# Performance work log

Measured on AMD Instinct MI355X. Metric: run time of the kernel, lower is better.

## Reference

```python
import jax, jax.numpy as jnp
import numpy as np

DIM = 1024
HEADS = 16
DIM_HEAD = 64
INNER = HEADS * DIM_HEAD  # 1024
SCALE = DIM_HEAD ** -0.5


def setup_inputs() -> dict:
    key = jax.random.key(0)
    ks = jax.random.split(key, 6)
    b, n = 4, 2048
    x = jax.random.normal(ks[0], (b, n, DIM), dtype=jnp.float32)
    gamma = jnp.ones((DIM,), dtype=jnp.float32)
    # weights stored (in, out); torch Linear computes x @ W.T with W (out, in)
    w_q = jax.random.normal(ks[1], (DIM, INNER), dtype=jnp.float32) * (DIM ** -0.5)
    w_kv = jax.random.normal(ks[2], (DIM, 2 * INNER), dtype=jnp.float32) * (DIM ** -0.5)
    w_out = jax.random.normal(ks[3], (INNER, DIM), dtype=jnp.float32) * (INNER ** -0.5)
    null_kv = jax.random.normal(ks[4], (2, HEADS, 1, DIM_HEAD), dtype=jnp.float32)
    return {"x": x, "gamma": gamma, "w_q": w_q, "w_kv": w_kv, "w_out": w_out, "null_kv": null_kv}


def _layer_norm(x, gamma):
    mu = jnp.mean(x, axis=-1, keepdims=True)
    var = jnp.var(x, axis=-1, keepdims=True)
    return (x - mu) * jax.lax.rsqrt(var + 1e-5) * gamma  # beta == 0


def reference(x, gamma, w_q, w_kv, w_out, null_kv):
    b, n, _ = x.shape
    xn = _layer_norm(x, gamma)
    q = xn @ w_q  # [b, n, inner]
    kv = xn @ w_kv
    k, v = jnp.split(kv, 2, axis=-1)
    q = q * SCALE

    def to_heads(t):
        return t.reshape(b, n, HEADS, DIM_HEAD).transpose(0, 2, 1, 3)  # b h n d

    q, k, v = map(to_heads, (q, k, v))
    nk = jnp.broadcast_to(null_kv[0][None], (b, HEADS, 1, DIM_HEAD))
    nv = jnp.broadcast_to(null_kv[1][None], (b, HEADS, 1, DIM_HEAD))
    k = jnp.concatenate([nk, k], axis=2)  # b h (n+1) d
    v = jnp.concatenate([nv, v], axis=2)
    sim = jnp.einsum('bhid,bhjd->bhij', q, k)
    attn = jax.nn.softmax(sim, axis=-1)
    out = jnp.einsum('bhij,bhjd->bhid', attn, v)
    out = out.transpose(0, 2, 1, 3).reshape(b, n, INNER)
    return out @ w_out
```

## Files before the change

kernel.cpp:

```cpp
#include <hip/hip_runtime.h>

typedef unsigned short ushort_t;
using f32x4   = __attribute__((ext_vector_type(4))) float;
using bf16x8  = __attribute__((ext_vector_type(8))) __bf16;
using bf16x4  = __attribute__((ext_vector_type(4))) __bf16;
using short4_t = __attribute__((ext_vector_type(4))) short;
using u32x2   = __attribute__((ext_vector_type(2))) unsigned;

typedef __attribute__((address_space(1))) const void gvoid_t;
typedef __attribute__((address_space(3))) void svoid_t;

union Frag {
    uint4    u4;
    bf16x8   b;
    ushort_t s[8];
};
union Frag2 {
    u32x2    u2;
    bf16x4   b;
    short4_t s4;
    unsigned u[2];
};

__device__ __forceinline__ ushort_t f2bf(float f) {
    union { float f; unsigned u; } a; a.f = f;
    unsigned u = a.u;
    unsigned r = (u + 0x7fffu + ((u >> 16) & 1u)) >> 16;
    return (ushort_t)r;
}
__device__ __forceinline__ float bf2f(ushort_t b) {
    union { unsigned u; float f; } a; a.u = ((unsigned)b) << 16;
    return a.f;
}
__device__ __forceinline__ unsigned pack2bf(float lo, float hi) {
    union { __bf16 h[2]; unsigned u; } p;
    p.h[0] = (__bf16)lo;
    p.h[1] = (__bf16)hi;
    return p.u;
}
__device__ __forceinline__ float exp2_fast(float x) {
#if __has_builtin(__builtin_amdgcn_exp2f)
    return __builtin_amdgcn_exp2f(x);
#else
    return exp2f(x);
#endif
}
__device__ __forceinline__ f32x4 mfma16(Frag2 a, Frag2 b, f32x4 c) {
#if __has_builtin(__builtin_amdgcn_mfma_f32_16x16x16_bf16)
    return __builtin_amdgcn_mfma_f32_16x16x16_bf16(a.b, b.b, c, 0, 0, 0);
#elif __has_builtin(__builtin_amdgcn_mfma_f32_16x16x16bf16_1k)
    return __builtin_amdgcn_mfma_f32_16x16x16bf16_1k(a.s4, b.s4, c, 0, 0, 0);
#else
    f32x4 d;
    asm("v_mfma_f32_16x16x16_bf16 %0, %1, %2, %3"
        : "=v"(d) : "v"(a.u2), "v"(b.u2), "v"(c));
    return d;
#endif
}

#define QSCALE 0.18033688011112042f

__global__ __launch_bounds__(256)
void ln_kernel(const float* __restrict__ x, const float* __restrict__ gamma,
               ushort_t* __restrict__ xn)
{
    const int row = blockIdx.x;
    const int tid = threadIdx.x;
    const float4 v = *reinterpret_cast<const float4*>(x + (size_t)row * 1024 + tid * 4);

    float s = v.x + v.y + v.z + v.w;
    float q = v.x * v.x + v.y * v.y + v.z * v.z + v.w * v.w;
    #pragma unroll
    for (int off = 1; off <= 32; off <<= 1) {
        s += __shfl_xor(s, off);
        q += __shfl_xor(q, off);
    }
    __shared__ float ss[4], sq[4];
    if ((tid & 63) == 0) { ss[tid >> 6] = s; sq[tid >> 6] = q; }
    __syncthreads();
    const float S  = ss[0] + ss[1] + ss[2] + ss[3];
    const float Q  = sq[0] + sq[1] + sq[2] + sq[3];
    const float mu = S * (1.0f / 1024.0f);
    const float var = Q * (1.0f / 1024.0f) - mu * mu;
    const float rstd = rsqrtf(var + 1e-5f);

    const float4 gm = *reinterpret_cast<const float4*>(gamma + tid * 4);
    ushort4 o;
    o.x = f2bf((v.x - mu) * rstd * gm.x);
    o.y = f2bf((v.y - mu) * rstd * gm.y);
    o.z = f2bf((v.z - mu) * rstd * gm.z);
    o.w = f2bf((v.w - mu) * rstd * gm.w);
    *reinterpret_cast<ushort4*>(xn + (size_t)row * 1024 + tid * 4) = o;
}

__global__ __launch_bounds__(256)
void wt_kernel(const float* __restrict__ w, ushort_t* __restrict__ wt, int K, int N)
{
    __shared__ float tile[32][33];
    const int n0 = blockIdx.x * 32, k0 = blockIdx.y * 32;
    const int tx = threadIdx.x, ty = threadIdx.y;
    #pragma unroll
    for (int i = 0; i < 4; ++i) {
        int r = ty + i * 8;
        tile[r][tx] = w[(size_t)(k0 + r) * N + n0 + tx];
    }
    __syncthreads();
    #pragma unroll
    for (int i = 0; i < 4; ++i) {
        int r = ty + i * 8;
        wt[(size_t)(n0 + r) * K + k0 + tx] = f2bf(tile[tx][r]);
    }
}

template<int MODE>
__global__ __launch_bounds__(256)
void gemm_kernel(const ushort_t* __restrict__ A, const ushort_t* __restrict__ Bt,
                 ushort_t* __restrict__ o16a, ushort_t* __restrict__ o16b,
                 float* __restrict__ o32)
{
    __shared__ ushort_t ldsA[128 * 64];
    __shared__ ushort_t ldsB[128 * 64];

    const int tid = threadIdx.x;
    const int m0 = blockIdx.x * 128, n0 = blockIdx.y * 128;
    const int w = tid >> 6, l = tid & 63, g = l >> 4, c = l & 15;
    const int wm = w >> 1, wn = w & 1;

    const ushort_t* asrc[4];
    const ushort_t* bsrc[4];
    #pragma unroll
    for (int j = 0; j < 4; ++j) {
        const int gidx = j * 256 + tid;
        const int row = gidx >> 3;
        const int sl  = (gidx & 7) ^ (row & 7);
        asrc[j] = A  + (size_t)(m0 + row) * 1024 + sl * 8;
        bsrc[j] = Bt + (size_t)(n0 + row) * 1024 + sl * 8;
    }

    f32x4 acc[4][4];
    #pragma unroll
    for (int mi = 0; mi < 4; ++mi)
        #pragma unroll
        for (int ni = 0; ni < 4; ++ni)
            acc[mi][ni] = (f32x4){0.f, 0.f, 0.f, 0.f};

    const int swz = c & 7;

    for (int kt = 0; kt < 16; ++kt) {
        if (kt) __syncthreads();
        #pragma unroll
        for (int j = 0; j < 4; ++j) {
            __builtin_amdgcn_global_load_lds((gvoid_t*)(asrc[j] + kt * 64),
                                             (svoid_t*)(&ldsA[(j * 256 + tid) * 8]), 16, 0, 0);
            __builtin_amdgcn_global_load_lds((gvoid_t*)(bsrc[j] + kt * 64),
                                             (svoid_t*)(&ldsB[(j * 256 + tid) * 8]), 16, 0, 0);
        }
        __syncthreads();

        #pragma unroll
        for (int kk = 0; kk < 2; ++kk) {
            Frag af[4], bfr[4];
            #pragma unroll
            for (int mi = 0; mi < 4; ++mi)
                af[mi].u4 = *reinterpret_cast<const uint4*>(
                    &ldsA[(wm * 64 + mi * 16 + c) * 64 + ((((kk << 2) | g)) ^ swz) * 8]);
            #pragma unroll
            for (int ni = 0; ni < 4; ++ni)
                bfr[ni].u4 = *reinterpret_cast<const uint4*>(
                    &ldsB[(wn * 64 + ni * 16 + c) * 64 + ((((kk << 2) | g)) ^ swz) * 8]);
            #pragma unroll
            for (int mi = 0; mi < 4; ++mi)
                #pragma unroll
                for (int ni = 0; ni < 4; ++ni)
                    acc[mi][ni] = __builtin_amdgcn_mfma_f32_16x16x32_bf16(
                        af[mi].b, bfr[ni].b, acc[mi][ni], 0, 0, 0);
        }
    }

    #pragma unroll
    for (int mi = 0; mi < 4; ++mi) {
        const int mbase = m0 + wm * 64 + mi * 16 + g * 4;
        #pragma unroll
        for (int ni = 0; ni < 4; ++ni) {
            const int n = n0 + wn * 64 + ni * 16 + c;
            if (MODE == 0) {
                const int hh = n >> 6, d = n & 63;
                #pragma unroll
                for (int r = 0; r < 4; ++r) {
                    const int m = mbase + r;
                    const int b = m >> 11, tok = m & 2047;
                    o16a[(((size_t)b * 16 + hh) * 2048 + tok) * 64 + d] =
                        f2bf(acc[mi][ni][r] * QSCALE);
                }
            } else if (MODE == 1) {
                if (n < 1024) {
                    const int hh = n >> 6, d = n & 63;
                    #pragma unroll
                    for (int r = 0; r < 4; ++r) {
                        const int m = mbase + r;
                        const int b = m >> 11, tok = m & 2047;
                        o16a[(((size_t)b * 16 + hh) * 2048 + tok) * 64 + d] =
                            f2bf(acc[mi][ni][r]);
                    }
                } else {
                    const int nn = n - 1024;
                    const int hh = nn >> 6, d = nn & 63;
                    const int b = mbase >> 11, tok0 = mbase & 2047;
                    ushort4 pv;
                    pv.x = f2bf(acc[mi][ni][0]);
                    pv.y = f2bf(acc[mi][ni][1]);
                    pv.z = f2bf(acc[mi][ni][2]);
                    pv.w = f2bf(acc[mi][ni][3]);
                    *reinterpret_cast<ushort4*>(
                        o16b + (((size_t)b * 16 + hh) * 64 + d) * 2048 + tok0) = pv;
                }
            } else {
                #pragma unroll
                for (int r = 0; r < 4; ++r)
                    o32[(size_t)(mbase + r) * 1024 + n] = acc[mi][ni][r];
            }
        }
    }
}

__global__ __launch_bounds__(512, 8)
void attn_kernel(const ushort_t* __restrict__ q, const ushort_t* __restrict__ k,
                 const ushort_t* __restrict__ vt, const float* __restrict__ nkv,
                 ushort_t* __restrict__ out)
{
    __shared__ ushort_t kvs[2][8192];

    const int tid = threadIdx.x;
    const int w = tid >> 6, l = tid & 63, g = l >> 4, c = l & 15;
    const int bh = blockIdx.x, qb = blockIdx.y, h = bh & 15;

    const ushort_t* kb = k  + (size_t)bh * 2048 * 64;
    const ushort_t* vb = vt + (size_t)bh * 64 * 2048;

    const int srow = tid >> 3;
    const int ssl  = (tid & 7) ^ (srow & 7);
    const ushort_t* ksrc = kb + srow * 64 + ssl * 8;
    const ushort_t* vsrc = vb + srow * 2048 + ssl * 8;

    const ushort_t* qbase = q + ((size_t)bh * 2048 + qb * 128 + w * 16) * 64;
    Frag aq[2];
    #pragma unroll
    for (int kk = 0; kk < 2; ++kk)
        aq[kk].u4 = *reinterpret_cast<const uint4*>(qbase + c * 64 + kk * 32 + g * 8);

    float snull = 0.f;
    #pragma unroll
    for (int kk = 0; kk < 2; ++kk) {
        const float4 n0 = *reinterpret_cast<const float4*>(nkv + h * 64 + kk * 32 + g * 8);
        const float4 n1 = *reinterpret_cast<const float4*>(nkv + h * 64 + kk * 32 + g * 8 + 4);
        snull += bf2f(aq[kk].s[0]) * n0.x + bf2f(aq[kk].s[1]) * n0.y
               + bf2f(aq[kk].s[2]) * n0.z + bf2f(aq[kk].s[3]) * n0.w;
        snull += bf2f(aq[kk].s[4]) * n1.x + bf2f(aq[kk].s[5]) * n1.y
               + bf2f(aq[kk].s[6]) * n1.z + bf2f(aq[kk].s[7]) * n1.w;
    }
    snull += __shfl_xor(snull, 16);
    snull += __shfl_xor(snull, 32);

    float m_run  = snull;
    float l_part = (l < 16) ? 1.f : 0.f;

    f32x4 acc[4];
    #pragma unroll
    for (int nf = 0; nf < 4; ++nf) {
        const float4 nv = *reinterpret_cast<const float4*>(nkv + 1024 + h * 64 + nf * 16 + g * 4);
        acc[nf] = (f32x4){nv.x, nv.y, nv.z, nv.w};
    }

    const int swz = c & 7;

    __builtin_amdgcn_global_load_lds((gvoid_t*)(ksrc), (svoid_t*)(&kvs[0][tid * 8]), 16, 0, 0);
    __builtin_amdgcn_global_load_lds((gvoid_t*)(vsrc), (svoid_t*)(&kvs[0][4096 + tid * 8]), 16, 0, 0);
    __syncthreads();

    int cur = 0;
    for (int t = 0; t < 32; ++t) {
        if (t < 31) {
            __builtin_amdgcn_global_load_lds((gvoid_t*)(ksrc + (t + 1) * 4096),
                                             (svoid_t*)(&kvs[cur ^ 1][tid * 8]), 16, 0, 0);
            __builtin_amdgcn_global_load_lds((gvoid_t*)(vsrc + (t + 1) * 64),
                                             (svoid_t*)(&kvs[cur ^ 1][4096 + tid * 8]), 16, 0, 0);
        }
        const ushort_t* kbuf = &kvs[cur][0];
        const ushort_t* vbuf = &kvs[cur][4096];

        f32x4 st[4];
        __builtin_amdgcn_s_setprio(1);
        #pragma unroll
        for (int nt = 0; nt < 4; ++nt) {
            Frag bk0, bk1;
            bk0.u4 = *reinterpret_cast<const uint4*>(
                &kbuf[(nt * 16 + c) * 64 + ((g) ^ swz) * 8]);
            bk1.u4 = *reinterpret_cast<const uint4*>(
                &kbuf[(nt * 16 + c) * 64 + ((4 | g) ^ swz) * 8]);
            f32x4 z = (f32x4){0.f, 0.f, 0.f, 0.f};
            st[nt] = __builtin_amdgcn_mfma_f32_16x16x32_bf16(bk0.b, aq[0].b, z, 0, 0, 0);
            st[nt] = __builtin_amdgcn_mfma_f32_16x16x32_bf16(bk1.b, aq[1].b, st[nt], 0, 0, 0);
        }
        __builtin_amdgcn_s_setprio(0);

        float m01 = fmaxf(fmaxf(st[0][0], st[0][1]), fmaxf(st[0][2], st[0][3]));
        float m23 = fmaxf(fmaxf(st[1][0], st[1][1]), fmaxf(st[1][2], st[1][3]));
        float m45 = fmaxf(fmaxf(st[2][0], st[2][1]), fmaxf(st[2][2], st[2][3]));
        float m67 = fmaxf(fmaxf(st[3][0], st[3][1]), fmaxf(st[3][2], st[3][3]));
        float pm = fmaxf(fmaxf(m01, m23), fmaxf(m45, m67));
        pm = fmaxf(pm, __shfl_xor(pm, 16));
        pm = fmaxf(pm, __shfl_xor(pm, 32));

        if (__any(pm > m_run + 12.f)) {
            const float nm = fmaxf(m_run, pm);
            const float alpha = exp2_fast(m_run - nm);
            m_run = nm;
            l_part *= alpha;
            #pragma unroll
            for (int nf = 0; nf < 4; ++nf)
                #pragma unroll
                for (int r = 0; r < 4; ++r)
                    acc[nf][r] *= alpha;
        }

        #pragma unroll
        for (int nt = 0; nt < 4; ++nt)
            #pragma unroll
            for (int r = 0; r < 4; ++r)
                st[nt][r] = exp2_fast(st[nt][r] - m_run);

        float s0 = (st[0][0] + st[0][1]) + (st[0][2] + st[0][3]);
        float s1 = (st[1][0] + st[1][1]) + (st[1][2] + st[1][3]);
        float s2 = (st[2][0] + st[2][1]) + (st[2][2] + st[2][3]);
        float s3 = (st[3][0] + st[3][1]) + (st[3][2] + st[3][3]);
        l_part += (s0 + s1) + (s2 + s3);

        Frag2 pb[4];
        #pragma unroll
        for (int nt = 0; nt < 4; ++nt) {
            pb[nt].u[0] = pack2bf(st[nt][0], st[nt][1]);
            pb[nt].u[1] = pack2bf(st[nt][2], st[nt][3]);
        }

        __builtin_amdgcn_s_setprio(1);
        #pragma unroll
        for (int nf = 0; nf < 4; ++nf) {
            const ushort_t* vrow = vbuf + (nf * 16 + c) * 64;
            #pragma unroll
            for (int nt = 0; nt < 4; ++nt) {
                Frag2 va;
                va.u2 = *reinterpret_cast<const u32x2*>(
                    &vrow[(((nt << 1) | (g >> 1)) ^ swz) * 8 + (g & 1) * 4]);
                acc[nf] = mfma16(va, pb[nt], acc[nf]);
            }
        }
        __builtin_amdgcn_s_setprio(0);

        __syncthreads();
        cur ^= 1;
    }

    l_part += __shfl_xor(l_part, 16);
    l_part += __shfl_xor(l_part, 32);
    const float inv = 1.f / l_part;

    ushort_t* ob = out + ((size_t)(bh >> 4) * 2048 + qb * 128 + w * 16 + c) * 1024 + h * 64;
    #pragma unroll
    for (int nf = 0; nf < 4; ++nf) {
        uint2 ov;
        ov.x = pack2bf(acc[nf][0] * inv, acc[nf][1] * inv);
        ov.y = pack2bf(acc[nf][2] * inv, acc[nf][3] * inv);
        *reinterpret_cast<uint2*>(ob + nf * 16 + g * 4) = ov;
    }
}

extern "C" void kernel_launch(void* const* d_in, const int* in_sizes, int n_in,
                              void* d_out, int out_size, void* d_ws, size_t ws_size,
                              hipStream_t stream)
{
    (void)in_sizes; (void)n_in; (void)out_size; (void)ws_size;
    const float* x     = (const float*)d_in[0];
    const float* gamma = (const float*)d_in[1];
    const float* w_q   = (const float*)d_in[2];
    const float* w_kv  = (const float*)d_in[3];
    const float* w_out = (const float*)d_in[4];
    const float* nkv   = (const float*)d_in[5];
    float* out = (float*)d_out;

    char* ws = (char*)d_ws;
    ushort_t* xn   = (ushort_t*)(ws);
    ushort_t* wqT  = (ushort_t*)(ws + 16777216);
    ushort_t* wkvT = (ushort_t*)(ws + 18874368);
    ushort_t* woT  = (ushort_t*)(ws + 23068672);
    ushort_t* qh   = (ushort_t*)(ws + 25165824);
    ushort_t* kh   = (ushort_t*)(ws + 41943040);
    ushort_t* vtb  = (ushort_t*)(ws + 58720256);
    ushort_t* ao   = xn;

    ln_kernel<<<dim3(8192), dim3(256), 0, stream>>>(x, gamma, xn);
    wt_kernel<<<dim3(32, 32), dim3(32, 8), 0, stream>>>(w_q,  wqT, 1024, 1024);
    wt_kernel<<<dim3(64, 32), dim3(32, 8), 0, stream>>>(w_kv, wkvT, 1024, 2048);
    wt_kernel<<<dim3(32, 32), dim3(32, 8), 0, stream>>>(w_out, woT, 1024, 1024);

    gemm_kernel<0><<<dim3(64, 8),  dim3(256), 0, stream>>>(xn, wqT,  qh, nullptr, nullptr);
    gemm_kernel<1><<<dim3(64, 16), dim3(256), 0, stream>>>(xn, wkvT, kh, vtb, nullptr);

    attn_kernel<<<dim3(64, 16), dim3(512), 0, stream>>>(qh, kh, vtb, nkv, ao);

    gemm_kernel<2><<<dim3(64, 8), dim3(256), 0, stream>>>(ao, woT, nullptr, nullptr, out);
}
```

Before: 256.5 us.

## Switch attention to 32x32x16 MFMA with 256-query blocks and LDS-staged output

Rewrites the attention inner loop to use 32x32x16 bf16 MFMA tiles, with 32 query rows per wave and 256 queries per block. This halves the grid and doubles K/V reuse per LDS tile. The P fragments are rearranged for the second MFMA with permlane32_swap instead of using the smaller 16x16x16 instruction. The output is staged through swizzled LDS so global stores are coalesced 16-byte rows. The cost is more registers per thread (the occupancy hint of 8 was dropped) and fewer blocks to fill the GPU.

```diff
diff --git a/kernel.cpp b/kernel.cpp
--- a/kernel.cpp
+++ b/kernel.cpp
@@ -2,10 +2,8 @@
 
 typedef unsigned short ushort_t;
 using f32x4   = __attribute__((ext_vector_type(4))) float;
+using f32x16  = __attribute__((ext_vector_type(16))) float;
 using bf16x8  = __attribute__((ext_vector_type(8))) __bf16;
-using bf16x4  = __attribute__((ext_vector_type(4))) __bf16;
-using short4_t = __attribute__((ext_vector_type(4))) short;
-using u32x2   = __attribute__((ext_vector_type(2))) unsigned;
 
 typedef __attribute__((address_space(1))) const void gvoid_t;
 typedef __attribute__((address_space(3))) void svoid_t;
@@ -14,12 +12,6 @@
     uint4    u4;
     bf16x8   b;
     ushort_t s[8];
-};
-union Frag2 {
-    u32x2    u2;
-    bf16x4   b;
-    short4_t s4;
-    unsigned u[2];
 };
 
 __device__ __forceinline__ ushort_t f2bf(float f) {
@@ -45,17 +37,16 @@
     return exp2f(x);
 #endif
 }
-__device__ __forceinline__ f32x4 mfma16(Frag2 a, Frag2 b, f32x4 c) {
-#if __has_builtin(__builtin_amdgcn_mfma_f32_16x16x16_bf16)
-    return __builtin_amdgcn_mfma_f32_16x16x16_bf16(a.b, b.b, c, 0, 0, 0);
-#elif __has_builtin(__builtin_amdgcn_mfma_f32_16x16x16bf16_1k)
-    return __builtin_amdgcn_mfma_f32_16x16x16bf16_1k(a.s4, b.s4, c, 0, 0, 0);
+__device__ __forceinline__ void pl32swap(unsigned &x, unsigned &y) {
+#if __has_builtin(__builtin_amdgcn_permlane32_swap)
+    auto r = __builtin_amdgcn_permlane32_swap((int)x, (int)y, false, false);
+    x = (unsigned)r[0]; y = (unsigned)r[1];
 #else
-    f32x4 d;
-    asm("v_mfma_f32_16x16x16_bf16 %0, %1, %2, %3"
-        : "=v"(d) : "v"(a.u2), "v"(b.u2), "v"(c));
-    return d;
+    asm volatile("v_permlane32_swap_b32 %0, %1" : "+v"(x), "+v"(y));
 #endif
+}
+__device__ __forceinline__ f32x16 mfma32(bf16x8 a, bf16x8 b, f32x16 c) {
+    return __builtin_amdgcn_mfma_f32_32x32x16_bf16(a, b, c, 0, 0, 0);
 }
 
 #define QSCALE 0.18033688011112042f
@@ -223,7 +214,7 @@
     }
 }
 
-__global__ __launch_bounds__(512, 8)
+__global__ __launch_bounds__(512)
 void attn_kernel(const ushort_t* __restrict__ q, const ushort_t* __restrict__ k,
                  const ushort_t* __restrict__ vt, const float* __restrict__ nkv,
                  ushort_t* __restrict__ out)
@@ -231,8 +222,9 @@
     __shared__ ushort_t kvs[2][8192];
 
     const int tid = threadIdx.x;
-    const int w = tid >> 6, l = tid & 63, g = l >> 4, c = l & 15;
-    const int bh = blockIdx.x, qb = blockIdx.y, h = bh & 15;
+    const int w = tid >> 6, l = tid & 63;
+    const int qc = l & 31, hh = l >> 5;
+    const int bh = blockIdx.x, qb = blockIdx.y, hd = bh & 15;
 
     const ushort_t* kb = k  + (size_t)bh * 2048 * 64;
     const ushort_t* vb = vt + (size_t)bh * 64 * 2048;
@@ -242,36 +234,35 @@
     const ushort_t* ksrc = kb + srow * 64 + ssl * 8;
     const ushort_t* vsrc = vb + srow * 2048 + ssl * 8;
 
-    const ushort_t* qbase = q + ((size_t)bh * 2048 + qb * 128 + w * 16) * 64;
-    Frag aq[2];
-    #pragma unroll
-    for (int kk = 0; kk < 2; ++kk)
-        aq[kk].u4 = *reinterpret_cast<const uint4*>(qbase + c * 64 + kk * 32 + g * 8);
+    const ushort_t* qbase = q + ((size_t)bh * 2048 + qb * 256 + w * 32 + qc) * 64;
+    Frag aq[4];
+    #pragma unroll
+    for (int dwin = 0; dwin < 4; ++dwin)
+        aq[dwin].u4 = *reinterpret_cast<const uint4*>(qbase + dwin * 16 + hh * 8);
 
     float snull = 0.f;
     #pragma unroll
-    for (int kk = 0; kk < 2; ++kk) {
-        const float4 n0 = *reinterpret_cast<const float4*>(nkv + h * 64 + kk * 32 + g * 8);
-        const float4 n1 = *reinterpret_cast<const float4*>(nkv + h * 64 + kk * 32 + g * 8 + 4);
-        snull += bf2f(aq[kk].s[0]) * n0.x + bf2f(aq[kk].s[1]) * n0.y
-               + bf2f(aq[kk].s[2]) * n0.z + bf2f(aq[kk].s[3]) * n0.w;
-        snull += bf2f(aq[kk].s[4]) * n1.x + bf2f(aq[kk].s[5]) * n1.y
-               + bf2f(aq[kk].s[6]) * n1.z + bf2f(aq[kk].s[7]) * n1.w;
-    }
-    snull += __shfl_xor(snull, 16);
+    for (int dwin = 0; dwin < 4; ++dwin) {
+        const float4 n0 = *reinterpret_cast<const float4*>(nkv + hd * 64 + dwin * 16 + hh * 8);
+        const float4 n1 = *reinterpret_cast<const float4*>(nkv + hd * 64 + dwin * 16 + hh * 8 + 4);
+        snull += bf2f(aq[dwin].s[0]) * n0.x + bf2f(aq[dwin].s[1]) * n0.y
+               + bf2f(aq[dwin].s[2]) * n0.z + bf2f(aq[dwin].s[3]) * n0.w;
+        snull += bf2f(aq[dwin].s[4]) * n1.x + bf2f(aq[dwin].s[5]) * n1.y
+               + bf2f(aq[dwin].s[6]) * n1.z + bf2f(aq[dwin].s[7]) * n1.w;
+    }
     snull += __shfl_xor(snull, 32);
 
     float m_run  = snull;
-    float l_part = (l < 16) ? 1.f : 0.f;
-
-    f32x4 acc[4];
-    #pragma unroll
-    for (int nf = 0; nf < 4; ++nf) {
-        const float4 nv = *reinterpret_cast<const float4*>(nkv + 1024 + h * 64 + nf * 16 + g * 4);
-        acc[nf] = (f32x4){nv.x, nv.y, nv.z, nv.w};
-    }
-
-    const int swz = c & 7;
+    float l_part = (hh == 0) ? 1.f : 0.f;
+
+    f32x16 acc[2];
+    #pragma unroll
+    for (int db = 0; db < 2; ++db)
+        #pragma unroll
+        for (int r = 0; r < 16; ++r)
+            acc[db][r] = nkv[1024 + hd * 64 + db * 32 + (r & 3) + 8 * (r >> 2) + 4 * hh];
+
+    const int swz = l & 7;
 
     __builtin_amdgcn_global_load_lds((gvoid_t*)(ksrc), (svoid_t*)(&kvs[0][tid * 8]), 16, 0, 0);
     __builtin_amdgcn_global_load_lds((gvoid_t*)(vsrc), (svoid_t*)(&kvs[0][4096 + tid * 8]), 16, 0, 0);
@@ -288,27 +279,27 @@
         const ushort_t* kbuf = &kvs[cur][0];
         const ushort_t* vbuf = &kvs[cur][4096];
 
-        f32x4 st[4];
+        f32x16 st[2];
         __builtin_amdgcn_s_setprio(1);
         #pragma unroll
-        for (int nt = 0; nt < 4; ++nt) {
-            Frag bk0, bk1;
-            bk0.u4 = *reinterpret_cast<const uint4*>(
-                &kbuf[(nt * 16 + c) * 64 + ((g) ^ swz) * 8]);
-            bk1.u4 = *reinterpret_cast<const uint4*>(
-                &kbuf[(nt * 16 + c) * 64 + ((4 | g) ^ swz) * 8]);
-            f32x4 z = (f32x4){0.f, 0.f, 0.f, 0.f};
-            st[nt] = __builtin_amdgcn_mfma_f32_16x16x32_bf16(bk0.b, aq[0].b, z, 0, 0, 0);
-            st[nt] = __builtin_amdgcn_mfma_f32_16x16x32_bf16(bk1.b, aq[1].b, st[nt], 0, 0, 0);
+        for (int kvblk = 0; kvblk < 2; ++kvblk) {
+            f32x16 z = {0.f,0.f,0.f,0.f, 0.f,0.f,0.f,0.f, 0.f,0.f,0.f,0.f, 0.f,0.f,0.f,0.f};
+            #pragma unroll
+            for (int dwin = 0; dwin < 4; ++dwin) {
+                Frag kf;
+                kf.u4 = *reinterpret_cast<const uint4*>(
+                    &kbuf[(kvblk * 32 + (l & 31)) * 64 + (((dwin << 1) | hh) ^ swz) * 8]);
+                z = mfma32(kf.b, aq[dwin].b, z);
+            }
+            st[kvblk] = z;
         }
         __builtin_amdgcn_s_setprio(0);
 
-        float m01 = fmaxf(fmaxf(st[0][0], st[0][1]), fmaxf(st[0][2], st[0][3]));
-        float m23 = fmaxf(fmaxf(st[1][0], st[1][1]), fmaxf(st[1][2], st[1][3]));
-        float m45 = fmaxf(fmaxf(st[2][0], st[2][1]), fmaxf(st[2][2], st[2][3]));
-        float m67 = fmaxf(fmaxf(st[3][0], st[3][1]), fmaxf(st[3][2], st[3][3]));
-        float pm = fmaxf(fmaxf(m01, m23), fmaxf(m45, m67));
-        pm = fmaxf(pm, __shfl_xor(pm, 16));
+        float pm = st[0][0];
+        #pragma unroll
+        for (int r = 1; r < 16; ++r) pm = fmaxf(pm, st[0][r]);
+        #pragma unroll
+        for (int r = 0; r < 16; ++r) pm = fmaxf(pm, st[1][r]);
         pm = fmaxf(pm, __shfl_xor(pm, 32));
 
         if (__any(pm > m_run + 12.f)) {
@@ -317,60 +308,83 @@
             m_run = nm;
             l_part *= alpha;
             #pragma unroll
-            for (int nf = 0; nf < 4; ++nf)
+            for (int db = 0; db < 2; ++db)
                 #pragma unroll
-                for (int r = 0; r < 4; ++r)
-                    acc[nf][r] *= alpha;
-        }
-
-        #pragma unroll
-        for (int nt = 0; nt < 4; ++nt)
-            #pragma unroll
-            for (int r = 0; r < 4; ++r)
-                st[nt][r] = exp2_fast(st[nt][r] - m_run);
-
-        float s0 = (st[0][0] + st[0][1]) + (st[0][2] + st[0][3]);
-        float s1 = (st[1][0] + st[1][1]) + (st[1][2] + st[1][3]);
-        float s2 = (st[2][0] + st[2][1]) + (st[2][2] + st[2][3]);
-        float s3 = (st[3][0] + st[3][1]) + (st[3][2] + st[3][3]);
-        l_part += (s0 + s1) + (s2 + s3);
-
-        Frag2 pb[4];
-        #pragma unroll
-        for (int nt = 0; nt < 4; ++nt) {
-            pb[nt].u[0] = pack2bf(st[nt][0], st[nt][1]);
-            pb[nt].u[1] = pack2bf(st[nt][2], st[nt][3]);
-        }
+                for (int r = 0; r < 16; ++r)
+                    acc[db][r] *= alpha;
+        }
+
+        float ts = 0.f;
+        #pragma unroll
+        for (int B = 0; B < 2; ++B)
+            #pragma unroll
+            for (int r = 0; r < 16; ++r) {
+                st[B][r] = exp2_fast(st[B][r] - m_run);
+                ts += st[B][r];
+            }
+        l_part += ts;
+
+        Frag pb[2][2];
+        #pragma unroll
+        for (int B = 0; B < 2; ++B)
+            #pragma unroll
+            for (int kbv = 0; kbv < 2; ++kbv) {
+                unsigned P = pack2bf(st[B][8 * kbv + 0], st[B][8 * kbv + 1]);
+                unsigned Q = pack2bf(st[B][8 * kbv + 2], st[B][8 * kbv + 3]);
+                unsigned R = pack2bf(st[B][8 * kbv + 4], st[B][8 * kbv + 5]);
+                unsigned S = pack2bf(st[B][8 * kbv + 6], st[B][8 * kbv + 7]);
+                pl32swap(P, R);
+                pl32swap(Q, S);
+                pb[B][kbv].u4.x = P;
+                pb[B][kbv].u4.y = Q;
+                pb[B][kbv].u4.z = R;
+                pb[B][kbv].u4.w = S;
+            }
 
         __builtin_amdgcn_s_setprio(1);
         #pragma unroll
-        for (int nf = 0; nf < 4; ++nf) {
-            const ushort_t* vrow = vbuf + (nf * 16 + c) * 64;
-            #pragma unroll
-            for (int nt = 0; nt < 4; ++nt) {
-                Frag2 va;
-                va.u2 = *reinterpret_cast<const u32x2*>(
-                    &vrow[(((nt << 1) | (g >> 1)) ^ swz) * 8 + (g & 1) * 4]);
-                acc[nf] = mfma16(va, pb[nt], acc[nf]);
-            }
-        }
+        for (int db = 0; db < 2; ++db)
+            #pragma unroll
+            for (int B = 0; B < 2; ++B)
+                #pragma unroll
+                for (int kbv = 0; kbv < 2; ++kbv) {
+                    Frag vf;
+                    vf.u4 = *reinterpret_cast<const uint4*>(
+                        &vbuf[(db * 32 + (l & 31)) * 64 + (((B << 2) | (kbv << 1) | hh) ^ swz) * 8]);
+                    acc[db] = mfma32(vf.b, pb[B][kbv].b, acc[db]);
+                }
         __builtin_amdgcn_s_setprio(0);
 
         __syncthreads();
         cur ^= 1;
     }
 
-    l_part += __shfl_xor(l_part, 16);
     l_part += __shfl_xor(l_part, 32);
     const float inv = 1.f / l_part;
 
-    ushort_t* ob = out + ((size_t)(bh >> 4) * 2048 + qb * 128 + w * 16 + c) * 1024 + h * 64;
-    #pragma unroll
-    for (int nf = 0; nf < 4; ++nf) {
-        uint2 ov;
-        ov.x = pack2bf(acc[nf][0] * inv, acc[nf][1] * inv);
-        ov.y = pack2bf(acc[nf][2] * inv, acc[nf][3] * inv);
-        *reinterpret_cast<uint2*>(ob + nf * 16 + g * 4) = ov;
+    ushort_t* olds = &kvs[0][0];
+    const int rowq = w * 32 + qc;
+    #pragma unroll
+    for (int db = 0; db < 2; ++db)
+        #pragma unroll
+        for (int rq = 0; rq < 4; ++rq) {
+            uint2 ov;
+            ov.x = pack2bf(acc[db][4 * rq + 0] * inv, acc[db][4 * rq + 1] * inv);
+            ov.y = pack2bf(acc[db][4 * rq + 2] * inv, acc[db][4 * rq + 3] * inv);
+            const int gL = db * 4 + rq;
+            const int phys = gL ^ (qc & 7);
+            *reinterpret_cast<uint2*>(&olds[(rowq * 8 + phys) * 8 + 4 * hh]) = ov;
+        }
+    __syncthreads();
+
+    const size_t obase = ((size_t)(bh >> 4) * 2048 + qb * 256) * 1024 + hd * 64;
+    #pragma unroll
+    for (int p = 0; p < 4; ++p) {
+        const int G = p * 512 + tid;
+        const int row = G >> 3, sl = G & 7;
+        const int phys = sl ^ (row & 7);
+        uint4 v = *reinterpret_cast<const uint4*>(&olds[(row * 8 + phys) * 8]);
+        *reinterpret_cast<uint4*>(out + obase + (size_t)row * 1024 + sl * 8) = v;
     }
 }
 
@@ -405,7 +419,7 @@
     gemm_kernel<0><<<dim3(64, 8),  dim3(256), 0, stream>>>(xn, wqT,  qh, nullptr, nullptr);
     gemm_kernel<1><<<dim3(64, 16), dim3(256), 0, stream>>>(xn, wkvT, kh, vtb, nullptr);
 
-    attn_kernel<<<dim3(64, 16), dim3(512), 0, stream>>>(qh, kh, vtb, nkv, ao);
+    attn_kernel<<<dim3(64, 8), dim3(512), 0, stream>>>(qh, kh, vtb, nkv, ao);
 
     gemm_kernel<2><<<dim3(64, 8), dim3(256), 0, stream>>>(ao, woT, nullptr, nullptr, out);
 }
```

Result: faster. 211.2 us (-17.7%).
